# Optimization experiments

Hardware: AMD Instinct MI355X
Metric: run time of the kernel (lower is better)

## Reference

```python
import jax, jax.numpy as jnp
import numpy as np

N_NODES = 100000
N_EDGES = 1600000
N_FEAT = 128
HIDDEN = 128
N_GRAPHS = 1024


def setup_inputs() -> dict:
    key = jax.random.key(0)
    ks = jax.random.split(key, 9)
    x = jax.random.normal(ks[0], (N_NODES, N_FEAT), dtype=jnp.float32)
    edge_index = jax.random.randint(ks[1], (2, N_EDGES), 0, N_NODES, dtype=jnp.int64)
    batch = jnp.sort(jax.random.randint(ks[2], (N_NODES,), 0, N_GRAPHS, dtype=jnp.int64))
    W1 = jax.random.normal(ks[3], (N_FEAT, HIDDEN), dtype=jnp.float32) * (1.0 / np.sqrt(N_FEAT))
    b1 = jax.random.normal(ks[4], (HIDDEN,), dtype=jnp.float32) * 0.01
    W2 = jax.random.normal(ks[5], (HIDDEN, HIDDEN), dtype=jnp.float32) * (1.0 / np.sqrt(HIDDEN))
    b2 = jax.random.normal(ks[6], (HIDDEN,), dtype=jnp.float32) * 0.01
    Wl = jax.random.normal(ks[7], (HIDDEN, 2), dtype=jnp.float32) * (1.0 / np.sqrt(HIDDEN))
    bl = jax.random.normal(ks[8], (2,), dtype=jnp.float32) * 0.01
    return {"x": x, "edge_index": edge_index, "batch": batch,
            "W1": W1, "b1": b1, "W2": W2, "b2": b2, "Wl": Wl, "bl": bl}


def _gcn_norm(edge_index, num_nodes):
    # PyG GCNConv: add self-loops, then sym-normalize with in-degree (target col).
    loop = jnp.arange(num_nodes, dtype=edge_index.dtype)
    src = jnp.concatenate([edge_index[0], loop])  # [E+N]
    dst = jnp.concatenate([edge_index[1], loop])  # [E+N]
    deg = jax.ops.segment_sum(jnp.ones_like(dst, dtype=jnp.float32), dst,
                              num_segments=num_nodes)
    dinv = jnp.where(deg > 0, jax.lax.rsqrt(deg), 0.0)
    norm = dinv[src] * dinv[dst]  # [E+N]
    return src, dst, norm


def _gcn_conv(h, W, b, src, dst, norm, num_nodes):
    h = h @ W                                   # [N, out]
    msg = h[src] * norm[:, None]                # gather + scale, [E+N, out]
    agg = jax.ops.segment_sum(msg, dst, num_segments=num_nodes)  # scatter-add
    return agg + b


def reference(x, edge_index, batch, W1, b1, W2, b2, Wl, bl):
    n = x.shape[0]
    src, dst, norm = _gcn_norm(edge_index, n)
    h = jax.nn.relu(_gcn_conv(x, W1, b1, src, dst, norm, n))
    h = jax.nn.relu(_gcn_conv(h, W2, b2, src, dst, norm, n))
    # global_mean_pool over graph ids
    sums = jax.ops.segment_sum(h, batch, num_segments=N_GRAPHS)        # [G, H]
    counts = jax.ops.segment_sum(jnp.ones((n,), jnp.float32), batch,
                                 num_segments=N_GRAPHS)
    pooled = sums / jnp.maximum(counts, 1.0)[:, None]
    # F.dropout with training=False default in inference -> identity
    return pooled @ Wl + bl  # [G, 2]
```

## Files before the change

### kernel.cpp

```cpp
#include <hip/hip_runtime.h>
#include <hip/hip_bf16.h>

#define N_NODES 100000
#define N_EDGES 1600000
#define FEAT 128
#define N_GRAPHS 1024
#define NBUCK 391
#define CHUNK 4096
#define NTILES 1563
#define G1A 781
#define G1B 782

typedef short short8 __attribute__((ext_vector_type(8)));
typedef float float4v __attribute__((ext_vector_type(4)));

static __device__ inline unsigned short f2bf(float f) {
    __hip_bfloat16 b = __float2bfloat16(f);
    unsigned short r;
    __builtin_memcpy(&r, &b, 2);
    return r;
}
static __device__ inline float bf_lo(unsigned int v) { return __uint_as_float(v << 16); }
static __device__ inline float bf_hi(unsigned int v) { return __uint_as_float(v & 0xFFFF0000u); }

__global__ __launch_bounds__(256) void k_prep_hist(const float* __restrict__ W1,
                                                   const float* __restrict__ W2,
                                                   unsigned short* __restrict__ wp1,
                                                   unsigned short* __restrict__ wp2,
                                                   const int* __restrict__ dst,
                                                   int* __restrict__ bcount,
                                                   unsigned int* __restrict__ udummy,
                                                   float* __restrict__ dinv) {
    int bid = blockIdx.x;
    if (bid < 128) {
        const float* W = (bid < 64) ? W1 : W2;
        unsigned short* wp = (bid < 64) ? wp1 : wp2;
        int t = (bid & 63) * 256 + threadIdx.x;
        int k = t >> 7, n = t & 127;
        float w = W[k * 128 + n];
        unsigned ub = __float_as_uint(w);
        unsigned short hi = (unsigned short)(ub >> 16);
        float hif = __uint_as_float(ub & 0xFFFF0000u);
        unsigned short lo = f2bf(w - hif);
        int sidx = n * 128 + ((k & 7) | (8 * (((k >> 3) ^ n) & 15)));
        wp[sidx] = hi;
        wp[16384 + sidx] = lo;
        if (bid == 0) {
            if (threadIdx.x < 64) udummy[threadIdx.x] = 0;
            if (threadIdx.x == 64) dinv[N_NODES] = 0.f;
        }
    } else {
        __shared__ int h[NBUCK];
        for (int i = threadIdx.x; i < NBUCK; i += 256) h[i] = 0;
        __syncthreads();
        int hb = bid - 128;
        for (int e = hb * 256 + threadIdx.x; e < N_EDGES; e += 256 * 256)
            atomicAdd(&h[dst[e] >> 8], 1);
        __syncthreads();
        for (int i = threadIdx.x; i < NBUCK; i += 256) {
            int c = h[i];
            if (c) atomicAdd(&bcount[i], c);
        }
    }
}

__global__ __launch_bounds__(512) void k_scan391(const int* __restrict__ in,
                                                 int* __restrict__ base,
                                                 int* __restrict__ cur,
                                                 int* __restrict__ tail) {
    int t = threadIdx.x;
    int v = (t < NBUCK) ? in[t] : 0;
    int lane = t & 63, wid = t >> 6;
    int s = v;
#pragma unroll
    for (int d = 1; d < 64; d <<= 1) { int n = __shfl_up(s, d); if (lane >= d) s += n; }
    __shared__ int ws[8];
    if (lane == 63) ws[wid] = s;
    __syncthreads();
    if (t < 8) {
        int x = ws[t];
#pragma unroll
        for (int d = 1; d < 8; d <<= 1) { int n = __shfl_up(x, d); if ((int)t >= d) x += n; }
        ws[t] = x;
    }
    __syncthreads();
    int excl = s - v + (wid ? ws[wid - 1] : 0);
    if (t < NBUCK) {
        base[t] = excl;
        cur[t] = excl;
    }
    if (t == 0) tail[0] = N_EDGES;
}

__device__ __forceinline__ void gemm_f32_body(int tile, const float* __restrict__ inp,
                                              const unsigned short* __restrict__ wp,
                                              unsigned short* __restrict__ u) {
    __shared__ unsigned short sW[32768];
    {
        float4* d4 = (float4*)sW;
        const float4* s4 = (const float4*)wp;
#pragma unroll
        for (int i = 0; i < 16; ++i) d4[threadIdx.x + 256 * i] = s4[threadIdx.x + 256 * i];
    }
    __syncthreads();
    const int t = threadIdx.x;
    const int wv = t >> 6, L = t & 63;
    const int m = L & 15, q = L >> 4;
    const int r0 = tile * 64 + wv * 16;
    int arow = r0 + m;
    if (arow >= N_NODES) arow = N_NODES - 1;
    const float4* ap = (const float4*)(inp + (size_t)arow * 128);
    float4v acc[8];
#pragma unroll
    for (int c = 0; c < 8; ++c) acc[c] = (float4v){0.f, 0.f, 0.f, 0.f};
#pragma unroll
    for (int k0 = 0; k0 < 128; k0 += 32) {
        float4 f0 = ap[(k0 >> 2) + 2 * q];
        float4 f1 = ap[(k0 >> 2) + 2 * q + 1];
        float fa[8] = {f0.x, f0.y, f0.z, f0.w, f1.x, f1.y, f1.z, f1.w};
        short8 ah, al;
#pragma unroll
        for (int j = 0; j < 8; ++j) {
            unsigned ub = __float_as_uint(fa[j]);
            ah[j] = (short)(ub >> 16);
            float hif = __uint_as_float(ub & 0xFFFF0000u);
            al[j] = (short)f2bf(fa[j] - hif);
        }
        const int b = (k0 >> 3) + q;
#pragma unroll
        for (int c = 0; c < 8; ++c) {
            int ng = c * 16 + m;
            int elem = ng * 128 + 8 * ((b ^ ng) & 15);
            short8 bh = *(const short8*)&sW[elem];
            short8 bl = *(const short8*)&sW[16384 + elem];
            acc[c] = __builtin_amdgcn_mfma_f32_16x16x32_bf16(ah, bh, acc[c], 0, 0, 0);
            acc[c] = __builtin_amdgcn_mfma_f32_16x16x32_bf16(al, bh, acc[c], 0, 0, 0);
            acc[c] = __builtin_amdgcn_mfma_f32_16x16x32_bf16(ah, bl, acc[c], 0, 0, 0);
        }
    }
#pragma unroll
    for (int r = 0; r < 4; ++r) {
        int row = r0 + 4 * q + r;
        if (row < N_NODES) {
            unsigned short* up = u + (size_t)row * 128 + m;
#pragma unroll
            for (int c = 0; c < 8; ++c) up[c * 16] = f2bf(acc[c][r]);
        }
    }
}

__global__ __launch_bounds__(256) void k_bucket_g1(const int* __restrict__ src,
                                                   const int* __restrict__ dst,
                                                   int* __restrict__ bcur,
                                                   unsigned int* __restrict__ pairs,
                                                   const float* __restrict__ x,
                                                   const unsigned short* __restrict__ wp1,
                                                   unsigned short* __restrict__ u) {
    if (blockIdx.x >= NBUCK) {
        gemm_f32_body(blockIdx.x - NBUCK, x, wp1, u);
        return;
    }
    __shared__ int cnt[NBUCK];
    __shared__ int basebuf[NBUCK];
    int t = threadIdx.x;
    int e0 = blockIdx.x * CHUNK;
    for (int i = t; i < NBUCK; i += 256) cnt[i] = 0;
    __syncthreads();
    unsigned pk[16]; int bk[16];
#pragma unroll
    for (int j = 0; j < 16; ++j) {
        int e = e0 + j * 256 + t;
        if (e < N_EDGES) {
            int s = src[e], d = dst[e];
            bk[j] = d >> 8;
            pk[j] = ((unsigned)s << 8) | (unsigned)(d & 255);
            atomicAdd(&cnt[bk[j]], 1);
        } else bk[j] = -1;
    }
    __syncthreads();
    for (int i = t; i < NBUCK; i += 256) {
        int c = cnt[i];
        basebuf[i] = c ? atomicAdd(&bcur[i], c) : 0;
        cnt[i] = 0;
    }
    __syncthreads();
#pragma unroll
    for (int j = 0; j < 16; ++j) {
        if (bk[j] >= 0) {
            int p = basebuf[bk[j]] + atomicAdd(&cnt[bk[j]], 1);
            pairs[p] = pk[j];
        }
    }
}

__global__ __launch_bounds__(256) void k_bfill_g1(const unsigned int* __restrict__ pairs,
                                                  const int* __restrict__ bbase,
                                                  const int* __restrict__ bcount,
                                                  float* __restrict__ dinv,
                                                  int* __restrict__ offs,
                                                  int* __restrict__ csr,
                                                  const float* __restrict__ x,
                                                  const unsigned short* __restrict__ wp1,
                                                  unsigned short* __restrict__ u) {
    if (blockIdx.x >= NBUCK) {
        gemm_f32_body(blockIdx.x - NBUCK + G1A, x, wp1, u);
        return;
    }
    __shared__ int degl[256];
    __shared__ int lcur[256];
    __shared__ int ws[4];
    int b = blockIdx.x, t = threadIdx.x;
    degl[t] = 0;
    __syncthreads();
    int s0 = bbase[b], n = bcount[b];
    for (int i = t; i < n; i += 256) atomicAdd(&degl[pairs[s0 + i] & 255u], 1);
    __syncthreads();
    int node = b * 256 + t;
    int dv = degl[t];
    if (node < N_NODES) dinv[node] = rsqrtf((float)(dv + 1));
    int lane = t & 63, wid = t >> 6;
    int s = dv;
#pragma unroll
    for (int d = 1; d < 64; d <<= 1) { int nn = __shfl_up(s, d); if (lane >= d) s += nn; }
    if (lane == 63) ws[wid] = s;
    __syncthreads();
    if (t < 4) {
        int xx = ws[t];
#pragma unroll
        for (int d = 1; d < 4; d <<= 1) { int nn = __shfl_up(xx, d); if ((int)t >= d) xx += nn; }
        ws[t] = xx;
    }
    __syncthreads();
    int excl = s - dv + (wid ? ws[wid - 1] : 0) + bbase[b];
    if (node < N_NODES) offs[node] = excl;
    lcur[t] = excl;
    __syncthreads();
    for (int i = t; i < n; i += 256) {
        unsigned pr = pairs[s0 + i];
        int p = atomicAdd(&lcur[pr & 255u], 1);
        csr[p] = (int)(pr >> 8);
    }
}

__global__ __launch_bounds__(256) void k_gemm_mfma_bf(const unsigned short* __restrict__ hh,
                                                      const unsigned short* __restrict__ hl,
                                                      const unsigned short* __restrict__ wp,
                                                      unsigned short* __restrict__ u) {
    __shared__ unsigned short sW[32768];
    {
        float4* d4 = (float4*)sW;
        const float4* s4 = (const float4*)wp;
#pragma unroll
        for (int i = 0; i < 16; ++i) d4[threadIdx.x + 256 * i] = s4[threadIdx.x + 256 * i];
    }
    __syncthreads();
    const int t = threadIdx.x;
    const int wv = t >> 6, L = t & 63;
    const int m = L & 15, q = L >> 4;
    const int r0 = blockIdx.x * 64 + wv * 16;
    int arow = r0 + m;
    if (arow >= N_NODES) arow = N_NODES - 1;
    const unsigned short* hhp = hh + (size_t)arow * 128 + 8 * q;
    const unsigned short* hlp = hl + (size_t)arow * 128 + 8 * q;
    float4v acc[8];
#pragma unroll
    for (int c = 0; c < 8; ++c) acc[c] = (float4v){0.f, 0.f, 0.f, 0.f};
#pragma unroll
    for (int k0 = 0; k0 < 128; k0 += 32) {
        short8 ah = *(const short8*)(hhp + k0);
        short8 al = *(const short8*)(hlp + k0);
        const int b = (k0 >> 3) + q;
#pragma unroll
        for (int c = 0; c < 8; ++c) {
            int ng = c * 16 + m;
            int elem = ng * 128 + 8 * ((b ^ ng) & 15);
            short8 bh = *(const short8*)&sW[elem];
            short8 bl = *(const short8*)&sW[16384 + elem];
            acc[c] = __builtin_amdgcn_mfma_f32_16x16x32_bf16(ah, bh, acc[c], 0, 0, 0);
            acc[c] = __builtin_amdgcn_mfma_f32_16x16x32_bf16(al, bh, acc[c], 0, 0, 0);
            acc[c] = __builtin_amdgcn_mfma_f32_16x16x32_bf16(ah, bl, acc[c], 0, 0, 0);
        }
    }
#pragma unroll
    for (int r = 0; r < 4; ++r) {
        int row = r0 + 4 * q + r;
        if (row < N_NODES) {
            unsigned short* up = u + (size_t)row * 128 + m;
#pragma unroll
            for (int c = 0; c < 8; ++c) up[c * 16] = f2bf(acc[c][r]);
        }
    }
}

__global__ __launch_bounds__(256) void k_agg(const unsigned int* __restrict__ u,
                                             const int* __restrict__ offs,
                                             const int* __restrict__ csr,
                                             const float* __restrict__ dinv,
                                             const float* __restrict__ bias,
                                             unsigned int* __restrict__ hhp,
                                             unsigned int* __restrict__ hlp,
                                             const float* __restrict__ Wl,
                                             float* __restrict__ pnode) {
    int wid = threadIdx.x >> 6;
    int lane = threadIdx.x & 63;
    int node = __builtin_amdgcn_readfirstlane(blockIdx.x * 4 + wid);
    if (node >= N_NODES) return;
    int p = __builtin_amdgcn_readfirstlane(offs[node]);
    int e = __builtin_amdgcn_readfirstlane(offs[node + 1]);
    float dsf = dinv[node];
    unsigned int self = u[(size_t)node * 64 + lane];
    float ax0 = dsf * bf_lo(self), ay0 = dsf * bf_hi(self);
    float ax1 = 0.f, ay1 = 0.f, ax2 = 0.f, ay2 = 0.f, ax3 = 0.f, ay3 = 0.f;
    float ax4 = 0.f, ay4 = 0.f, ax5 = 0.f, ay5 = 0.f, ax6 = 0.f, ay6 = 0.f;
    float ax7 = 0.f, ay7 = 0.f;
    for (; p < e; p += 8) {
        int c0 = csr[p + 0], c1 = csr[p + 1], c2 = csr[p + 2], c3 = csr[p + 3];
        int c4 = csr[p + 4], c5 = csr[p + 5], c6 = csr[p + 6], c7 = csr[p + 7];
        int i0 = c0;
        int i1 = (p + 1 < e) ? c1 : N_NODES;
        int i2 = (p + 2 < e) ? c2 : N_NODES;
        int i3 = (p + 3 < e) ? c3 : N_NODES;
        int i4 = (p + 4 < e) ? c4 : N_NODES;
        int i5 = (p + 5 < e) ? c5 : N_NODES;
        int i6 = (p + 6 < e) ? c6 : N_NODES;
        int i7 = (p + 7 < e) ? c7 : N_NODES;
        float d0 = dinv[i0], d1 = dinv[i1], d2 = dinv[i2], d3 = dinv[i3];
        float d4 = dinv[i4], d5 = dinv[i5], d6 = dinv[i6], d7 = dinv[i7];
        unsigned v0 = (u + (size_t)i0 * 64)[lane];
        unsigned v1 = (u + (size_t)i1 * 64)[lane];
        unsigned v2 = (u + (size_t)i2 * 64)[lane];
        unsigned v3 = (u + (size_t)i3 * 64)[lane];
        unsigned v4 = (u + (size_t)i4 * 64)[lane];
        unsigned v5 = (u + (size_t)i5 * 64)[lane];
        unsigned v6 = (u + (size_t)i6 * 64)[lane];
        unsigned v7 = (u + (size_t)i7 * 64)[lane];
        ax0 = fmaf(d0, bf_lo(v0), ax0); ay0 = fmaf(d0, bf_hi(v0), ay0);
        ax1 = fmaf(d1, bf_lo(v1), ax1); ay1 = fmaf(d1, bf_hi(v1), ay1);
        ax2 = fmaf(d2, bf_lo(v2), ax2); ay2 = fmaf(d2, bf_hi(v2), ay2);
        ax3 = fmaf(d3, bf_lo(v3), ax3); ay3 = fmaf(d3, bf_hi(v3), ay3);
        ax4 = fmaf(d4, bf_lo(v4), ax4); ay4 = fmaf(d4, bf_hi(v4), ay4);
        ax5 = fmaf(d5, bf_lo(v5), ax5); ay5 = fmaf(d5, bf_hi(v5), ay5);
        ax6 = fmaf(d6, bf_lo(v6), ax6); ay6 = fmaf(d6, bf_hi(v6), ay6);
        ax7 = fmaf(d7, bf_lo(v7), ax7); ay7 = fmaf(d7, bf_hi(v7), ay7);
    }
    float2 b = ((const float2*)bias)[lane];
    float sx = ((ax0 + ax1) + (ax2 + ax3)) + ((ax4 + ax5) + (ax6 + ax7));
    float sy = ((ay0 + ay1) + (ay2 + ay3)) + ((ay4 + ay5) + (ay6 + ay7));
    float r0 = fmaxf(dsf * sx + b.x, 0.f);
    float r1 = fmaxf(dsf * sy + b.y, 0.f);
    if (hlp) {
        unsigned u0 = __float_as_uint(r0), u1 = __float_as_uint(r1);
        unsigned short h0 = (unsigned short)(u0 >> 16), h1 = (unsigned short)(u1 >> 16);
        float rf0 = __uint_as_float(u0 & 0xFFFF0000u), rf1 = __uint_as_float(u1 & 0xFFFF0000u);
        unsigned short l0 = f2bf(r0 - rf0), l1 = f2bf(r1 - rf1);
        hhp[(size_t)node * 64 + lane] = (unsigned)h0 | ((unsigned)h1 << 16);
        hlp[(size_t)node * 64 + lane] = (unsigned)l0 | ((unsigned)l1 << 16);
    } else {
        float2 wl0 = ((const float2*)Wl)[2 * lane];
        float2 wl1 = ((const float2*)Wl)[2 * lane + 1];
        float p0 = r0 * wl0.x + r1 * wl1.x;
        float p1 = r0 * wl0.y + r1 * wl1.y;
#pragma unroll
        for (int d = 32; d > 0; d >>= 1) {
            p0 += __shfl_xor(p0, d);
            p1 += __shfl_xor(p1, d);
        }
        if (lane == 0) {
            float2* pp = (float2*)pnode;
            pp[node] = (float2){p0, p1};
        }
    }
}

__global__ __launch_bounds__(64) void k_fin(const float* __restrict__ pnode,
                                            const int* __restrict__ batch,
                                            const float* __restrict__ bl,
                                            float* __restrict__ out) {
    int g = blockIdx.x;
    int lane = threadIdx.x;
    __shared__ int sb[2];
    if (lane < 2) {
        int tgt = g + lane;
        int lo = 0, hi = N_NODES;
        while (lo < hi) { int m = (lo + hi) >> 1; if (batch[m] < tgt) lo = m + 1; else hi = m; }
        sb[lane] = lo;
    }
    __syncthreads();
    int s0 = sb[0], s1 = sb[1];
    const float2* pp = (const float2*)pnode;
    float p0 = 0.f, p1 = 0.f;
    for (int i = s0 + lane; i < s1; i += 64) {
        float2 v = pp[i];
        p0 += v.x;
        p1 += v.y;
    }
#pragma unroll
    for (int d = 32; d > 0; d >>= 1) {
        p0 += __shfl_xor(p0, d);
        p1 += __shfl_xor(p1, d);
    }
    if (lane == 0) {
        float inv = 1.f / fmaxf((float)(s1 - s0), 1.f);
        out[2 * g + 0] = p0 * inv + bl[0];
        out[2 * g + 1] = p1 * inv + bl[1];
    }
}

extern "C" void kernel_launch(void* const* d_in, const int* in_sizes, int n_in,
                              void* d_out, int out_size, void* d_ws, size_t ws_size,
                              hipStream_t stream) {
    const float* x  = (const float*)d_in[0];
    const int* ei   = (const int*)d_in[1];
    const int* batch = (const int*)d_in[2];
    const float* W1 = (const float*)d_in[3];
    const float* b1 = (const float*)d_in[4];
    const float* W2 = (const float*)d_in[5];
    const float* b2 = (const float*)d_in[6];
    const float* Wl = (const float*)d_in[7];
    const float* bl = (const float*)d_in[8];
    float* out = (float*)d_out;
    const int* src = ei;
    const int* dst = ei + N_EDGES;

    char* ws = (char*)d_ws;
    size_t o = 0;
    auto alloc = [&](size_t bytes) -> void* {
        o = (o + 255) & ~(size_t)255;
        void* p = ws + o;
        o += bytes;
        return p;
    };
    int* bcount = (int*)alloc((size_t)NBUCK * 4);
    int* bbase  = (int*)alloc((size_t)NBUCK * 4);
    int* bcur   = (int*)alloc((size_t)NBUCK * 4);
    float* dinv = (float*)alloc((size_t)(N_NODES + 1) * 4);
    int* offs   = (int*)alloc((size_t)(N_NODES + 1) * 4);
    unsigned short* wp1 = (unsigned short*)alloc(65536);
    unsigned short* wp2 = (unsigned short*)alloc(65536);
    float* pnode = (float*)alloc((size_t)N_NODES * 2 * 4);
    unsigned int* pairs = (unsigned int*)alloc((size_t)N_EDGES * 4);
    int* csr    = (int*)alloc((size_t)(N_EDGES + 8) * 4);
    unsigned short* u = (unsigned short*)alloc((size_t)(N_NODES + 1) * 128 * 2);
    unsigned short* hh = (unsigned short*)alloc((size_t)N_NODES * 128 * 2);
    unsigned short* hl = (unsigned short*)alloc((size_t)N_NODES * 128 * 2);

    hipMemsetAsync(bcount, 0, (size_t)NBUCK * 4, stream);
    k_prep_hist<<<384, 256, 0, stream>>>(W1, W2, wp1, wp2, dst, bcount,
                                         (unsigned int*)(u + (size_t)N_NODES * 128), dinv);
    k_scan391<<<1, 512, 0, stream>>>(bcount, bbase, bcur, &offs[N_NODES]);
    k_bucket_g1<<<NBUCK + G1A, 256, 0, stream>>>(src, dst, bcur, pairs, x, wp1, u);
    k_bfill_g1<<<NBUCK + G1B, 256, 0, stream>>>(pairs, bbase, bcount, dinv, offs, csr, x, wp1, u);

    k_agg<<<(N_NODES + 3) / 4, 256, 0, stream>>>((const unsigned int*)u, offs, csr, dinv, b1,
                                                 (unsigned int*)hh, (unsigned int*)hl,
                                                 nullptr, nullptr);
    k_gemm_mfma_bf<<<NTILES, 256, 0, stream>>>(hh, hl, wp2, u);
    k_agg<<<(N_NODES + 3) / 4, 256, 0, stream>>>((const unsigned int*)u, offs, csr, dinv, b2,
                                                 nullptr, nullptr, Wl, pnode);

    k_fin<<<N_GRAPHS, 64, 0, stream>>>(pnode, batch, bl, out);
}
```

Measured before the change: 321.2 us.

## Fuse layer-1 aggregation with layer-2 GEMM through shared memory

Merges the first aggregation kernel and the second MFMA GEMM into one kernel. Each 512-thread block aggregates 32 nodes into a swizzled fp32 LDS tile, splits it into bf16 hi/lo on the fly, and multiplies by W2 held in LDS. This drops the hh/hl global round trip and one launch, and writes to a separate u2 buffer so other blocks' gathers from u are not disturbed. In exchange, each block loads the full 64KB W2 into LDS for only 32 rows, and the larger LDS footprint lowers occupancy for the latency-bound gather phase.

```diff
diff --git a/kernel.cpp b/kernel.cpp
--- a/kernel.cpp
+++ b/kernel.cpp
@@ -30,6 +30,7 @@
                                                    const int* __restrict__ dst,
                                                    int* __restrict__ bcount,
                                                    unsigned int* __restrict__ udummy,
+                                                   unsigned int* __restrict__ u2dummy,
                                                    float* __restrict__ dinv) {
     int bid = blockIdx.x;
     if (bid < 128) {
@@ -47,7 +48,8 @@
         wp[16384 + sidx] = lo;
         if (bid == 0) {
             if (threadIdx.x < 64) udummy[threadIdx.x] = 0;
-            if (threadIdx.x == 64) dinv[N_NODES] = 0.f;
+            else if (threadIdx.x < 128) u2dummy[threadIdx.x - 64] = 0;
+            else if (threadIdx.x == 128) dinv[N_NODES] = 0.f;
         }
     } else {
         __shared__ int h[NBUCK];
@@ -242,65 +244,127 @@
     }
 }
 
-__global__ __launch_bounds__(256) void k_gemm_mfma_bf(const unsigned short* __restrict__ hh,
-                                                      const unsigned short* __restrict__ hl,
-                                                      const unsigned short* __restrict__ wp,
-                                                      unsigned short* __restrict__ u) {
+__global__ __launch_bounds__(512) void k_agg1_g2(const unsigned int* __restrict__ u,
+                                                 const int* __restrict__ offs,
+                                                 const int* __restrict__ csr,
+                                                 const float* __restrict__ dinv,
+                                                 const float* __restrict__ bias,
+                                                 const unsigned short* __restrict__ wp,
+                                                 unsigned short* __restrict__ u2) {
     __shared__ unsigned short sW[32768];
+    __shared__ float hS[32 * 128];
     {
         float4* d4 = (float4*)sW;
         const float4* s4 = (const float4*)wp;
 #pragma unroll
-        for (int i = 0; i < 16; ++i) d4[threadIdx.x + 256 * i] = s4[threadIdx.x + 256 * i];
-    }
-    __syncthreads();
-    const int t = threadIdx.x;
-    const int wv = t >> 6, L = t & 63;
-    const int m = L & 15, q = L >> 4;
-    const int r0 = blockIdx.x * 64 + wv * 16;
-    int arow = r0 + m;
-    if (arow >= N_NODES) arow = N_NODES - 1;
-    const unsigned short* hhp = hh + (size_t)arow * 128 + 8 * q;
-    const unsigned short* hlp = hl + (size_t)arow * 128 + 8 * q;
-    float4v acc[8];
-#pragma unroll
-    for (int c = 0; c < 8; ++c) acc[c] = (float4v){0.f, 0.f, 0.f, 0.f};
+        for (int i = 0; i < 8; ++i) d4[threadIdx.x + 512 * i] = s4[threadIdx.x + 512 * i];
+    }
+    const int w = threadIdx.x >> 6;
+    const int lane = threadIdx.x & 63;
+    const int base = blockIdx.x * 32;
+
+    for (int n = 0; n < 4; ++n) {
+        const int row = 4 * w + n;
+        const int node = base + row;
+        int p = __builtin_amdgcn_readfirstlane(offs[node]);
+        int e = __builtin_amdgcn_readfirstlane(offs[node + 1]);
+        float dsf = dinv[node];
+        unsigned int self = u[(size_t)node * 64 + lane];
+        float ax0 = dsf * bf_lo(self), ay0 = dsf * bf_hi(self);
+        float ax1 = 0.f, ay1 = 0.f, ax2 = 0.f, ay2 = 0.f, ax3 = 0.f, ay3 = 0.f;
+        float ax4 = 0.f, ay4 = 0.f, ax5 = 0.f, ay5 = 0.f, ax6 = 0.f, ay6 = 0.f;
+        float ax7 = 0.f, ay7 = 0.f;
+        for (; p < e; p += 8) {
+            int c0 = csr[p + 0], c1 = csr[p + 1], c2 = csr[p + 2], c3 = csr[p + 3];
+            int c4 = csr[p + 4], c5 = csr[p + 5], c6 = csr[p + 6], c7 = csr[p + 7];
+            int i0 = c0;
+            int i1 = (p + 1 < e) ? c1 : N_NODES;
+            int i2 = (p + 2 < e) ? c2 : N_NODES;
+            int i3 = (p + 3 < e) ? c3 : N_NODES;
+            int i4 = (p + 4 < e) ? c4 : N_NODES;
+            int i5 = (p + 5 < e) ? c5 : N_NODES;
+            int i6 = (p + 6 < e) ? c6 : N_NODES;
+            int i7 = (p + 7 < e) ? c7 : N_NODES;
+            float d0 = dinv[i0], d1 = dinv[i1], d2 = dinv[i2], d3 = dinv[i3];
+            float d4 = dinv[i4], d5 = dinv[i5], d6 = dinv[i6], d7 = dinv[i7];
+            unsigned v0 = (u + (size_t)i0 * 64)[lane];
+            unsigned v1 = (u + (size_t)i1 * 64)[lane];
+            unsigned v2 = (u + (size_t)i2 * 64)[lane];
+            unsigned v3 = (u + (size_t)i3 * 64)[lane];
+            unsigned v4 = (u + (size_t)i4 * 64)[lane];
+            unsigned v5 = (u + (size_t)i5 * 64)[lane];
+            unsigned v6 = (u + (size_t)i6 * 64)[lane];
+            unsigned v7 = (u + (size_t)i7 * 64)[lane];
+            ax0 = fmaf(d0, bf_lo(v0), ax0); ay0 = fmaf(d0, bf_hi(v0), ay0);
+            ax1 = fmaf(d1, bf_lo(v1), ax1); ay1 = fmaf(d1, bf_hi(v1), ay1);
+            ax2 = fmaf(d2, bf_lo(v2), ax2); ay2 = fmaf(d2, bf_hi(v2), ay2);
+            ax3 = fmaf(d3, bf_lo(v3), ax3); ay3 = fmaf(d3, bf_hi(v3), ay3);
+            ax4 = fmaf(d4, bf_lo(v4), ax4); ay4 = fmaf(d4, bf_hi(v4), ay4);
+            ax5 = fmaf(d5, bf_lo(v5), ax5); ay5 = fmaf(d5, bf_hi(v5), ay5);
+            ax6 = fmaf(d6, bf_lo(v6), ax6); ay6 = fmaf(d6, bf_hi(v6), ay6);
+            ax7 = fmaf(d7, bf_lo(v7), ax7); ay7 = fmaf(d7, bf_hi(v7), ay7);
+        }
+        float2 b = ((const float2*)bias)[lane];
+        float sx = ((ax0 + ax1) + (ax2 + ax3)) + ((ax4 + ax5) + (ax6 + ax7));
+        float sy = ((ay0 + ay1) + (ay2 + ay3)) + ((ay4 + ay5) + (ay6 + ay7));
+        float r0 = fmaxf(dsf * sx + b.x, 0.f);
+        float r1 = fmaxf(dsf * sy + b.y, 0.f);
+        int g4 = (lane >> 1) ^ (row & 7);
+        float2* hp = (float2*)&hS[row * 128 + g4 * 4 + (lane & 1) * 2];
+        *hp = (float2){r0, r1};
+    }
+    __syncthreads();
+
+    const int m = lane & 15, q = lane >> 4;
+    const int rt = w >> 2;
+    const int cw = w & 3;
+    const int arow = 16 * rt + m;
+    float4v acc[2];
+    acc[0] = (float4v){0.f, 0.f, 0.f, 0.f};
+    acc[1] = (float4v){0.f, 0.f, 0.f, 0.f};
 #pragma unroll
     for (int k0 = 0; k0 < 128; k0 += 32) {
-        short8 ah = *(const short8*)(hhp + k0);
-        short8 al = *(const short8*)(hlp + k0);
+        int g1 = (k0 >> 2) + 2 * q;
+        float4 f0 = *(const float4*)&hS[arow * 128 + ((g1 ^ (arow & 7)) << 2)];
+        float4 f1 = *(const float4*)&hS[arow * 128 + (((g1 + 1) ^ (arow & 7)) << 2)];
+        float fa[8] = {f0.x, f0.y, f0.z, f0.w, f1.x, f1.y, f1.z, f1.w};
+        short8 ah, al;
+#pragma unroll
+        for (int j = 0; j < 8; ++j) {
+            unsigned ub = __float_as_uint(fa[j]);
+            ah[j] = (short)(ub >> 16);
+            float hif = __uint_as_float(ub & 0xFFFF0000u);
+            al[j] = (short)f2bf(fa[j] - hif);
+        }
         const int b = (k0 >> 3) + q;
 #pragma unroll
-        for (int c = 0; c < 8; ++c) {
+        for (int cc = 0; cc < 2; ++cc) {
+            int c = 2 * cw + cc;
             int ng = c * 16 + m;
             int elem = ng * 128 + 8 * ((b ^ ng) & 15);
             short8 bh = *(const short8*)&sW[elem];
             short8 bl = *(const short8*)&sW[16384 + elem];
-            acc[c] = __builtin_amdgcn_mfma_f32_16x16x32_bf16(ah, bh, acc[c], 0, 0, 0);
-            acc[c] = __builtin_amdgcn_mfma_f32_16x16x32_bf16(al, bh, acc[c], 0, 0, 0);
-            acc[c] = __builtin_amdgcn_mfma_f32_16x16x32_bf16(ah, bl, acc[c], 0, 0, 0);
+            acc[cc] = __builtin_amdgcn_mfma_f32_16x16x32_bf16(ah, bh, acc[cc], 0, 0, 0);
+            acc[cc] = __builtin_amdgcn_mfma_f32_16x16x32_bf16(al, bh, acc[cc], 0, 0, 0);
+            acc[cc] = __builtin_amdgcn_mfma_f32_16x16x32_bf16(ah, bl, acc[cc], 0, 0, 0);
         }
     }
 #pragma unroll
     for (int r = 0; r < 4; ++r) {
-        int row = r0 + 4 * q + r;
-        if (row < N_NODES) {
-            unsigned short* up = u + (size_t)row * 128 + m;
-#pragma unroll
-            for (int c = 0; c < 8; ++c) up[c * 16] = f2bf(acc[c][r]);
-        }
-    }
-}
-
-__global__ __launch_bounds__(256) void k_agg(const unsigned int* __restrict__ u,
-                                             const int* __restrict__ offs,
-                                             const int* __restrict__ csr,
-                                             const float* __restrict__ dinv,
-                                             const float* __restrict__ bias,
-                                             unsigned int* __restrict__ hhp,
-                                             unsigned int* __restrict__ hlp,
-                                             const float* __restrict__ Wl,
-                                             float* __restrict__ pnode) {
+        int row = 16 * rt + 4 * q + r;
+        unsigned short* up = u2 + (size_t)(base + row) * 128 + m;
+        up[(2 * cw + 0) * 16] = f2bf(acc[0][r]);
+        up[(2 * cw + 1) * 16] = f2bf(acc[1][r]);
+    }
+}
+
+__global__ __launch_bounds__(256) void k_agg2(const unsigned int* __restrict__ u,
+                                              const int* __restrict__ offs,
+                                              const int* __restrict__ csr,
+                                              const float* __restrict__ dinv,
+                                              const float* __restrict__ bias,
+                                              const float* __restrict__ Wl,
+                                              float* __restrict__ pnode) {
     int wid = threadIdx.x >> 6;
     int lane = threadIdx.x & 63;
     int node = __builtin_amdgcn_readfirstlane(blockIdx.x * 4 + wid);
@@ -348,27 +412,18 @@
     float sy = ((ay0 + ay1) + (ay2 + ay3)) + ((ay4 + ay5) + (ay6 + ay7));
     float r0 = fmaxf(dsf * sx + b.x, 0.f);
     float r1 = fmaxf(dsf * sy + b.y, 0.f);
-    if (hlp) {
-        unsigned u0 = __float_as_uint(r0), u1 = __float_as_uint(r1);
-        unsigned short h0 = (unsigned short)(u0 >> 16), h1 = (unsigned short)(u1 >> 16);
-        float rf0 = __uint_as_float(u0 & 0xFFFF0000u), rf1 = __uint_as_float(u1 & 0xFFFF0000u);
-        unsigned short l0 = f2bf(r0 - rf0), l1 = f2bf(r1 - rf1);
-        hhp[(size_t)node * 64 + lane] = (unsigned)h0 | ((unsigned)h1 << 16);
-        hlp[(size_t)node * 64 + lane] = (unsigned)l0 | ((unsigned)l1 << 16);
-    } else {
-        float2 wl0 = ((const float2*)Wl)[2 * lane];
-        float2 wl1 = ((const float2*)Wl)[2 * lane + 1];
-        float p0 = r0 * wl0.x + r1 * wl1.x;
-        float p1 = r0 * wl0.y + r1 * wl1.y;
-#pragma unroll
-        for (int d = 32; d > 0; d >>= 1) {
-            p0 += __shfl_xor(p0, d);
-            p1 += __shfl_xor(p1, d);
-        }
-        if (lane == 0) {
-            float2* pp = (float2*)pnode;
-            pp[node] = (float2){p0, p1};
-        }
+    float2 wl0 = ((const float2*)Wl)[2 * lane];
+    float2 wl1 = ((const float2*)Wl)[2 * lane + 1];
+    float p0 = r0 * wl0.x + r1 * wl1.x;
+    float p1 = r0 * wl0.y + r1 * wl1.y;
+#pragma unroll
+    for (int d = 32; d > 0; d >>= 1) {
+        p0 += __shfl_xor(p0, d);
+        p1 += __shfl_xor(p1, d);
+    }
+    if (lane == 0) {
+        float2* pp = (float2*)pnode;
+        pp[node] = (float2){p0, p1};
     }
 }
 
@@ -440,23 +495,21 @@
     float* pnode = (float*)alloc((size_t)N_NODES * 2 * 4);
     unsigned int* pairs = (unsigned int*)alloc((size_t)N_EDGES * 4);
     int* csr    = (int*)alloc((size_t)(N_EDGES + 8) * 4);
-    unsigned short* u = (unsigned short*)alloc((size_t)(N_NODES + 1) * 128 * 2);
-    unsigned short* hh = (unsigned short*)alloc((size_t)N_NODES * 128 * 2);
-    unsigned short* hl = (unsigned short*)alloc((size_t)N_NODES * 128 * 2);
+    unsigned short* u  = (unsigned short*)alloc((size_t)(N_NODES + 1) * 128 * 2);
+    unsigned short* u2 = (unsigned short*)alloc((size_t)(N_NODES + 1) * 128 * 2);
 
     hipMemsetAsync(bcount, 0, (size_t)NBUCK * 4, stream);
     k_prep_hist<<<384, 256, 0, stream>>>(W1, W2, wp1, wp2, dst, bcount,
-                                         (unsigned int*)(u + (size_t)N_NODES * 128), dinv);
+                                         (unsigned int*)(u + (size_t)N_NODES * 128),
+                                         (unsigned int*)(u2 + (size_t)N_NODES * 128), dinv);
     k_scan391<<<1, 512, 0, stream>>>(bcount, bbase, bcur, &offs[N_NODES]);
     k_bucket_g1<<<NBUCK + G1A, 256, 0, stream>>>(src, dst, bcur, pairs, x, wp1, u);
     k_bfill_g1<<<NBUCK + G1B, 256, 0, stream>>>(pairs, bbase, bcount, dinv, offs, csr, x, wp1, u);
 
-    k_agg<<<(N_NODES + 3) / 4, 256, 0, stream>>>((const unsigned int*)u, offs, csr, dinv, b1,
-                                                 (unsigned int*)hh, (unsigned int*)hl,
-                                                 nullptr, nullptr);
-    k_gemm_mfma_bf<<<NTILES, 256, 0, stream>>>(hh, hl, wp2, u);
-    k_agg<<<(N_NODES + 3) / 4, 256, 0, stream>>>((const unsigned int*)u, offs, csr, dinv, b2,
-                                                 nullptr, nullptr, Wl, pnode);
+    k_agg1_g2<<<N_NODES / 32, 512, 0, stream>>>((const unsigned int*)u, offs, csr, dinv, b1,
+                                                wp2, u2);
+    k_agg2<<<(N_NODES + 3) / 4, 256, 0, stream>>>((const unsigned int*)u2, offs, csr, dinv, b2,
+                                                  Wl, pnode);
 
     k_fin<<<N_GRAPHS, 64, 0, stream>>>(pnode, batch, bl, out);
 }
```

Measured after the change: 319.3 us. About the same (-0.6%).
